# Performance work log

Measured on AMD Instinct MI355X. Metric: run time of the kernel, lower is better.

The kernel has to match this reference:

```python
import jax, jax.numpy as jnp
import numpy as np

# Complete 4-ary tree, leaves at depth 8, heap layout (children of i are 4i+1..4i+4).
B_ARY = 4
DEPTH = 8          # depths 0..8, leaves at depth 8
H = 512            # hidden_channels
IN = 512           # in_channels
OUT = 256          # out_channels
L = 2              # num_layers
LEVEL_STARTS = np.array([(B_ARY ** d - 1) // (B_ARY - 1) for d in range(DEPTH + 2)])
N = int(LEVEL_STARTS[-1])  # 87381


def setup_inputs() -> dict:
    key = jax.random.key(0)
    ks = jax.random.split(key, 12)
    x = jax.random.normal(ks[0], (N, IN), jnp.float32)

    # tree structure (numpy, deterministic)
    n_internal = int(LEVEL_STARTS[DEPTH])
    child_idx = np.zeros((N, B_ARY), np.int32)
    child_mask = np.zeros((N, B_ARY), np.int32)
    internal = np.arange(n_internal)
    child_idx[:n_internal] = (internal[:, None] * B_ARY + 1 + np.arange(B_ARY)[None, :]).astype(np.int32)
    child_mask[:n_internal] = 1
    node_parent = np.full(N, -1, np.int64)
    node_parent[1:] = (np.arange(1, N) - 1) // B_ARY
    node_depth = np.zeros(N, np.int64)
    for d in range(DEPTH + 1):
        node_depth[LEVEL_STARTS[d]:LEVEL_STARTS[d + 1]] = d
    is_leaf = node_depth == DEPTH
    edge_index = np.stack([np.arange(1, N), node_parent[1:]]).astype(np.int64)
    batch = np.zeros(N, np.int64)

    s = 0.02
    params = dict(
        W_in=jax.random.normal(ks[1], (IN, H), jnp.float32) * s,
        b_in=jnp.zeros((H,), jnp.float32),
        W_ioux=jax.random.normal(ks[2], (L, H, 3 * H), jnp.float32) * s,
        b_ioux=jnp.zeros((L, 3 * H), jnp.float32),
        W_iouh=jax.random.normal(ks[3], (L, H, 3 * H), jnp.float32) * s,
        b_iouh=jnp.zeros((L, 3 * H), jnp.float32),
        W_fx=jax.random.normal(ks[4], (L, H, H), jnp.float32) * s,
        b_fx=jnp.zeros((L, H), jnp.float32),
        W_fh=jax.random.normal(ks[5], (L, H, H), jnp.float32) * s,
        b_fh=jnp.zeros((L, H), jnp.float32),
        W_out=jax.random.normal(ks[6], (H, OUT), jnp.float32) * s,
        b_out=jnp.zeros((OUT,), jnp.float32),
    )
    return dict(
        x=x,
        edge_index=jnp.asarray(edge_index),
        batch=jnp.asarray(batch),
        node_depth=jnp.asarray(node_depth),
        node_parent=jnp.asarray(node_parent),
        is_leaf=jnp.asarray(is_leaf),
        child_idx=jnp.asarray(child_idx),
        child_mask=jnp.asarray(child_mask),
        **params,
    )


def reference(x, edge_index, batch, node_depth, node_parent, is_leaf,
              child_idx, child_mask,
              W_in, b_in, W_ioux, b_ioux, W_iouh, b_iouh,
              W_fx, b_fx, W_fh, b_fh, W_out, b_out):
    cm = child_mask.astype(x.dtype)  # [N, B]
    h = jax.nn.relu(x @ W_in + b_in)  # input projection (dropout = eval mode identity)
    for l in range(L):
        hidden = jnp.zeros((N, H), x.dtype)
        cell = jnp.zeros((N, H), x.dtype)
        # bottom-up over tree levels; levels are contiguous static slices
        for d in range(DEPTH, -1, -1):
            s, e = int(LEVEL_STARTS[d]), int(LEVEL_STARTS[d + 1])
            xl = h[s:e]                                   # [n_d, H]
            ci = child_idx[s:e]                           # [n_d, B]
            m = cm[s:e][..., None]                        # [n_d, B, 1]
            ch = hidden[ci] * m                           # masked child hidden
            cc = cell[ci] * m                             # masked child cell
            h_sum = ch.sum(axis=1)                        # child-sum
            iou = xl @ W_ioux[l] + b_ioux[l] + h_sum @ W_iouh[l] + b_iouh[l]
            i, o, u = jnp.split(iou, 3, axis=-1)
            i = jax.nn.sigmoid(i)
            o = jax.nn.sigmoid(o)
            u = jnp.tanh(u)
            f = jax.nn.sigmoid((xl @ W_fx[l] + b_fx[l])[:, None, :] + ch @ W_fh[l] + b_fh[l])
            c = i * u + (f * cc).sum(axis=1)
            hl = o * jnp.tanh(c)
            hidden = hidden.at[s:e].set(hl)
            cell = cell.at[s:e].set(c)
        h = hidden
    node_emb = h @ W_out + b_out                          # [N, OUT]
    tree_emb = jax.ops.segment_sum(node_emb, batch, num_segments=1)  # 'sum' aggregation
    return node_emb, tree_emb
```

## Files before the change

### kernel.cpp

```cpp
#include <hip/hip_runtime.h>

typedef __bf16 bf16;
typedef __bf16 bf16x8 __attribute__((ext_vector_type(8)));
typedef float f32x4 __attribute__((ext_vector_type(4)));

#define NN 87381
#define NINT 21845
#define NLEAF 65536
#define LEAF_START 21845

__device__ __forceinline__ float sigmoidf_(float x) {
    return 1.0f / (1.0f + __expf(-x));
}
__device__ __forceinline__ float tanhf_(float x) {
    return 1.0f - 2.0f / (__expf(2.0f * x) + 1.0f);
}

__device__ __forceinline__ void gload_lds16(const bf16* g, bf16* l) {
    __builtin_amdgcn_global_load_lds(
        (const __attribute__((address_space(1))) unsigned int*)g,
        (__attribute__((address_space(3))) unsigned int*)l, 16, 0, 0);
}

__device__ __forceinline__ int xcd_swz(int bid, int nwg) {
    int q = nwg >> 3, r = nwg & 7;
    int x = bid & 7, i = bid >> 3;
    return (x < r ? x * (q + 1) : r * (q + 1) + (x - r) * q) + i;
}

#define SWZ(r, kc) ((((r) << 3) | ((kc) ^ ((r) & 7))) << 3)

__global__ void tconv_kernel(const float* __restrict__ W, bf16* __restrict__ Wt,
                             int NR, int total) {
    int idx = blockIdx.x * 256 + threadIdx.x;
    if (idx >= total) return;
    int n = idx >> 9;
    int k = idx & 511;
    Wt[idx] = (bf16)W[(size_t)k * NR + n];
}

__global__ void convx_kernel(const float* __restrict__ X, bf16* __restrict__ Y, int total4) {
    int idx = blockIdx.x * 256 + threadIdx.x;
    if (idx >= total4) return;
    const float4 f = *reinterpret_cast<const float4*>(X + (size_t)idx * 4);
    bf16 o[4] = {(bf16)f.x, (bf16)f.y, (bf16)f.z, (bf16)f.w};
    *reinterpret_cast<ushort2*>(Y + (size_t)idx * 4 + 0) = *reinterpret_cast<ushort2*>(&o[0]);
    *reinterpret_cast<ushort2*>(Y + (size_t)idx * 4 + 2) = *reinterpret_cast<ushort2*>(&o[2]);
}

#define MFMA_COMPUTE_2x4(As, Bs, acc, wm, wn, lm, quad)                          \
    _Pragma("unroll")                                                            \
    for (int kk = 0; kk < 64; kk += 32) {                                        \
        const int kc_ = (kk >> 3) + quad;                                        \
        bf16x8 areg[2], breg[4];                                                 \
        _Pragma("unroll")                                                        \
        for (int mi = 0; mi < 2; ++mi)                                           \
            areg[mi] = *reinterpret_cast<const bf16x8*>(                         \
                &(As)[SWZ(wm + mi * 16 + lm, kc_)]);                             \
        _Pragma("unroll")                                                        \
        for (int ni = 0; ni < 4; ++ni)                                           \
            breg[ni] = *reinterpret_cast<const bf16x8*>(                         \
                &(Bs)[SWZ(wn + ni * 16 + lm, kc_)]);                             \
        _Pragma("unroll")                                                        \
        for (int mi = 0; mi < 2; ++mi)                                           \
            _Pragma("unroll")                                                    \
            for (int ni = 0; ni < 4; ++ni)                                       \
                acc[mi][ni] = __builtin_amdgcn_mfma_f32_16x16x32_bf16(           \
                    areg[mi], breg[ni], acc[mi][ni], 0, 0, 0);                   \
    }

__global__ __launch_bounds__(512)
void gemm_kernel(const bf16* __restrict__ A, const bf16* __restrict__ Bt,
                 int bstride, int K, int ntiles,
                 float* __restrict__ Cf, bf16* __restrict__ Cb,
                 const float* __restrict__ bias1, const float* __restrict__ bias2,
                 int M, int N, int relu, int swz)
{
    __shared__ __align__(16) bf16 As[2][128 * 64];
    __shared__ __align__(16) bf16 Bs[2][128 * 64];
    const int tid  = threadIdx.x;
    const int wave = tid >> 6;
    const int lane = tid & 63;
    int bid = blockIdx.x;
    if (swz) bid = xcd_swz(bid, (int)gridDim.x);
    const int bm = (bid / ntiles) * 128;
    const int bn = (bid % ntiles) * 128;
    const int wm = (wave & 3) * 32;
    const int wn = (wave >> 2) * 64;
    const int lm   = lane & 15;
    const int quad = lane >> 4;

    f32x4 acc[2][4];
#pragma unroll
    for (int i = 0; i < 2; ++i)
#pragma unroll
        for (int j = 0; j < 4; ++j) acc[i][j] = (f32x4){0.f, 0.f, 0.f, 0.f};

    const bf16* aptr[2];
    const bf16* bptr[2];
    int loff[2];
#pragma unroll
    for (int i = 0; i < 2; ++i) {
        int c   = i * 512 + tid;
        int r   = c >> 3;
        int kc8 = ((c & 7) ^ (r & 7)) << 3;
        int gr  = bm + r; gr = (gr < M) ? gr : (M - 1);
        aptr[i] = A + (size_t)gr * K + kc8;
        bptr[i] = Bt + (size_t)(bn + r) * bstride + kc8;
        loff[i] = c << 3;
    }

    auto stage = [&](int buf, int t) {
        const int kofs = t << 6;
#pragma unroll
        for (int i = 0; i < 2; ++i)
            gload_lds16(aptr[i] + kofs, &As[0][0] + buf * (128 * 64) + loff[i]);
#pragma unroll
        for (int i = 0; i < 2; ++i)
            gload_lds16(bptr[i] + kofs, &Bs[0][0] + buf * (128 * 64) + loff[i]);
    };

    const int nk = K >> 6;
    stage(0, 0);
    __syncthreads();
    int cur = 0;
    for (int t = 0; t < nk; ++t) {
        if (t + 1 < nk) stage(cur ^ 1, t + 1);
        MFMA_COMPUTE_2x4(As[cur], Bs[cur], acc, wm, wn, lm, quad);
        __syncthreads();
        cur ^= 1;
    }

#pragma unroll
    for (int ni = 0; ni < 4; ++ni) {
        int col = bn + wn + ni * 16 + lm;
        float bsum = (bias1 ? bias1[col] : 0.f) + (bias2 ? bias2[col] : 0.f);
#pragma unroll
        for (int mi = 0; mi < 2; ++mi) {
#pragma unroll
            for (int r = 0; r < 4; ++r) {
                int row = bm + wm + mi * 16 + quad * 4 + r;
                if (row < M) {
                    float v = acc[mi][ni][r] + bsum;
                    if (relu) v = (v > 0.f) ? v : 0.f;
                    if (Cf) Cf[(size_t)row * N + col] = v;
                    else    Cb[(size_t)row * N + col] = (bf16)v;
                }
            }
        }
    }
}

__global__ __launch_bounds__(512)
void leaf_kernel(const bf16* __restrict__ A, const bf16* __restrict__ wiou,
                 const float* __restrict__ bx1, const float* __restrict__ bx2,
                 bf16* __restrict__ hout, bf16* __restrict__ cellout,
                 bf16* __restrict__ hsout, int M, int swz)
{
    __shared__ __align__(16) bf16 As[2][128 * 64];
    __shared__ __align__(16) bf16 Bs[2][3 * 64 * 64];
    const int tid  = threadIdx.x;
    const int wave = tid >> 6;
    const int lane = tid & 63;
    int bid = blockIdx.x;
    if (swz) bid = xcd_swz(bid, (int)gridDim.x);
    const int bm = (bid >> 3) * 128;
    const int bn = (bid & 7) * 64;
    if (bm >= M) return;
    const int wm   = (wave & 3) * 32;
    const int wn   = (wave >> 2) * 32;
    const int lm   = lane & 15;
    const int quad = lane >> 4;

    f32x4 acc[3][2][2];
#pragma unroll
    for (int g = 0; g < 3; ++g)
#pragma unroll
        for (int i = 0; i < 2; ++i)
#pragma unroll
            for (int j = 0; j < 2; ++j) acc[g][i][j] = (f32x4){0.f, 0.f, 0.f, 0.f};

    const bf16* aptr[2];
    int aoff[2];
#pragma unroll
    for (int i = 0; i < 2; ++i) {
        int c   = i * 512 + tid;
        int r   = c >> 3;
        int kc8 = ((c & 7) ^ (r & 7)) << 3;
        int gr  = bm + r; gr = (gr < M) ? gr : (M - 1);
        aptr[i] = A + ((size_t)gr << 9) + kc8;
        aoff[i] = c << 3;
    }
    const bf16* bptr[3];
    int boff[3];
#pragma unroll
    for (int i = 0; i < 3; ++i) {
        int c   = i * 512 + tid;
        int g   = c >> 9;
        int cg  = c & 511;
        int r   = cg >> 3;
        int kc8 = ((cg & 7) ^ (r & 7)) << 3;
        bptr[i] = wiou + (size_t)(g * 512 + bn + r) * 512 + kc8;
        boff[i] = c << 3;
    }

    auto stage = [&](int buf, int t) {
        const int kofs = t << 6;
#pragma unroll
        for (int i = 0; i < 2; ++i)
            gload_lds16(aptr[i] + kofs, &As[0][0] + buf * (128 * 64) + aoff[i]);
#pragma unroll
        for (int i = 0; i < 3; ++i)
            gload_lds16(bptr[i] + kofs, &Bs[0][0] + buf * (3 * 64 * 64) + boff[i]);
    };

    stage(0, 0);
    __syncthreads();
    int cur = 0;
    for (int t = 0; t < 8; ++t) {
        if (t + 1 < 8) stage(cur ^ 1, t + 1);
#pragma unroll
        for (int kk = 0; kk < 64; kk += 32) {
            const int kc_ = (kk >> 3) + quad;
            bf16x8 areg[2];
#pragma unroll
            for (int mi = 0; mi < 2; ++mi)
                areg[mi] = *reinterpret_cast<const bf16x8*>(
                    &As[cur][SWZ(wm + mi * 16 + lm, kc_)]);
            bf16x8 breg[3][2];
#pragma unroll
            for (int g = 0; g < 3; ++g)
#pragma unroll
                for (int ni = 0; ni < 2; ++ni)
                    breg[g][ni] = *reinterpret_cast<const bf16x8*>(
                        &Bs[cur][g * 4096 + SWZ(wn + ni * 16 + lm, kc_)]);
#pragma unroll
            for (int g = 0; g < 3; ++g)
#pragma unroll
                for (int mi = 0; mi < 2; ++mi)
#pragma unroll
                    for (int ni = 0; ni < 2; ++ni)
                        acc[g][mi][ni] = __builtin_amdgcn_mfma_f32_16x16x32_bf16(
                            areg[mi], breg[g][ni], acc[g][mi][ni], 0, 0, 0);
        }
        __syncthreads();
        cur ^= 1;
    }

#pragma unroll
    for (int ni = 0; ni < 2; ++ni) {
        int col = bn + wn + ni * 16 + lm;
        float bi = bx1[col]        + bx2[col];
        float bo = bx1[col + 512]  + bx2[col + 512];
        float bu = bx1[col + 1024] + bx2[col + 1024];
#pragma unroll
        for (int mi = 0; mi < 2; ++mi) {
            int rbase = bm + wm + mi * 16 + quad * 4;
            float hsum = 0.f;
#pragma unroll
            for (int r = 0; r < 4; ++r) {
                int row = rbase + r;
                if (row < M) {
                    float i_ = sigmoidf_(acc[0][mi][ni][r] + bi);
                    float o_ = sigmoidf_(acc[1][mi][ni][r] + bo);
                    float u_ = tanhf_(acc[2][mi][ni][r] + bu);
                    float c  = i_ * u_;
                    bf16 hb  = (bf16)(o_ * tanhf_(c));
                    cellout[(size_t)row * 512 + col] = (bf16)c;
                    hout[(size_t)row * 512 + col] = hb;
                    hsum += (float)hb;
                }
            }
            if (hsout && rbase < M)
                hsout[(size_t)(rbase >> 2) * 512 + col] = (bf16)hsum;
        }
    }
}

__global__ __launch_bounds__(512)
void iou_fused_kernel(const bf16* __restrict__ A, const bf16* __restrict__ wiou,
                      const float* __restrict__ bx1, const float* __restrict__ bx2,
                      const float* __restrict__ fcs, const bf16* __restrict__ xout,
                      bf16* __restrict__ hout, bf16* __restrict__ cellout,
                      bf16* __restrict__ hsout,
                      int M, int swz)
{
    __shared__ __align__(16) bf16 As[2][128 * 64];
    __shared__ __align__(16) bf16 Bs[2][3 * 64 * 64];
    const int tid  = threadIdx.x;
    const int wave = tid >> 6;
    const int lane = tid & 63;
    int bid = blockIdx.x;
    if (swz) bid = xcd_swz(bid, (int)gridDim.x);
    const int bm = (bid >> 3) * 128;
    const int bn = (bid & 7) * 64;
    if (bm >= M) return;
    const int wm   = (wave & 3) * 32;
    const int wn   = (wave >> 2) * 32;
    const int lm   = lane & 15;
    const int quad = lane >> 4;

    f32x4 acc[3][2][2];
#pragma unroll
    for (int g = 0; g < 3; ++g)
#pragma unroll
        for (int i = 0; i < 2; ++i)
#pragma unroll
            for (int j = 0; j < 2; ++j) acc[g][i][j] = (f32x4){0.f, 0.f, 0.f, 0.f};

    const bf16* aptr[2];
    int aoff[2];
#pragma unroll
    for (int i = 0; i < 2; ++i) {
        int c   = i * 512 + tid;
        int r   = c >> 3;
        int kc8 = ((c & 7) ^ (r & 7)) << 3;
        int gr  = bm + r; gr = (gr < M) ? gr : (M - 1);
        aptr[i] = A + ((size_t)gr << 9) + kc8;
        aoff[i] = c << 3;
    }
    const bf16* bptr[3];
    int boff[3];
#pragma unroll
    for (int i = 0; i < 3; ++i) {
        int c   = i * 512 + tid;
        int g   = c >> 9;
        int cg  = c & 511;
        int r   = cg >> 3;
        int kc8 = ((cg & 7) ^ (r & 7)) << 3;
        bptr[i] = wiou + (size_t)(g * 512 + bn + r) * 512 + kc8;
        boff[i] = c << 3;
    }

    auto stage = [&](int buf, int t) {
        const int kofs = t << 6;
#pragma unroll
        for (int i = 0; i < 2; ++i)
            gload_lds16(aptr[i] + kofs, &As[0][0] + buf * (128 * 64) + aoff[i]);
#pragma unroll
        for (int i = 0; i < 3; ++i)
            gload_lds16(bptr[i] + kofs, &Bs[0][0] + buf * (3 * 64 * 64) + boff[i]);
    };

    stage(0, 0);
    __syncthreads();
    int cur = 0;
    for (int t = 0; t < 8; ++t) {
        if (t + 1 < 8) stage(cur ^ 1, t + 1);
#pragma unroll
        for (int kk = 0; kk < 64; kk += 32) {
            const int kc_ = (kk >> 3) + quad;
            bf16x8 areg[2];
#pragma unroll
            for (int mi = 0; mi < 2; ++mi)
                areg[mi] = *reinterpret_cast<const bf16x8*>(
                    &As[cur][SWZ(wm + mi * 16 + lm, kc_)]);
            bf16x8 breg[3][2];
#pragma unroll
            for (int g = 0; g < 3; ++g)
#pragma unroll
                for (int ni = 0; ni < 2; ++ni)
                    breg[g][ni] = *reinterpret_cast<const bf16x8*>(
                        &Bs[cur][g * 4096 + SWZ(wn + ni * 16 + lm, kc_)]);
#pragma unroll
            for (int g = 0; g < 3; ++g)
#pragma unroll
                for (int mi = 0; mi < 2; ++mi)
#pragma unroll
                    for (int ni = 0; ni < 2; ++ni)
                        acc[g][mi][ni] = __builtin_amdgcn_mfma_f32_16x16x32_bf16(
                            areg[mi], breg[g][ni], acc[g][mi][ni], 0, 0, 0);
        }
        __syncthreads();
        cur ^= 1;
    }

#pragma unroll
    for (int ni = 0; ni < 2; ++ni) {
        int col = bn + wn + ni * 16 + lm;
        float bi = bx1[col]        + bx2[col];
        float bo = bx1[col + 512]  + bx2[col + 512];
        float bu = bx1[col + 1024] + bx2[col + 1024];
#pragma unroll
        for (int mi = 0; mi < 2; ++mi) {
            int rbase = bm + wm + mi * 16 + quad * 4;
            float hsum = 0.f;
#pragma unroll
            for (int r = 0; r < 4; ++r) {
                int row = rbase + r;
                if (row < M) {
                    float ax  = (float)xout[(size_t)row * 2048 + col];
                    float aox = (float)xout[(size_t)row * 2048 + 512 + col];
                    float aux = (float)xout[(size_t)row * 2048 + 1024 + col];
                    float i_ = sigmoidf_(acc[0][mi][ni][r] + ax + bi);
                    float o_ = sigmoidf_(acc[1][mi][ni][r] + aox + bo);
                    float u_ = tanhf_(acc[2][mi][ni][r] + aux + bu);
                    float c  = i_ * u_ + fcs[(size_t)row * 512 + col];
                    bf16 hb  = (bf16)(o_ * tanhf_(c));
                    cellout[(size_t)row * 512 + col] = (bf16)c;
                    hout[(size_t)row * 512 + col] = hb;
                    hsum += (float)hb;
                }
            }
            if (hsout && rbase < M)
                hsout[(size_t)(rbase >> 2) * 512 + col] = (bf16)hsum;
        }
    }
}

__global__ __launch_bounds__(512)
void cf_kernel(const bf16* __restrict__ hc, const bf16* __restrict__ cellc,
               const bf16* __restrict__ wfh, const bf16* __restrict__ xout,
               const float* __restrict__ bf1, const float* __restrict__ bf2,
               float* __restrict__ fcs, int E, int swz)
{
    const int M = 4 * E;
    __shared__ __align__(16) bf16 As[2][128 * 64];
    __shared__ __align__(16) bf16 Bs[2][128 * 64];
    const int tid  = threadIdx.x;
    const int wave = tid >> 6;
    const int lane = tid & 63;
    int bid = blockIdx.x;
    if (swz) bid = xcd_swz(bid, (int)gridDim.x);
    const int bm = (bid >> 2) * 128;
    const int bn = (bid & 3) * 128;
    if (bm >= M) return;
    const int wm   = (wave & 3) * 32;
    const int wn   = (wave >> 2) * 64;
    const int lm   = lane & 15;
    const int quad = lane >> 4;

    f32x4 acc[2][4];
#pragma unroll
    for (int i = 0; i < 2; ++i)
#pragma unroll
        for (int j = 0; j < 4; ++j) acc[i][j] = (f32x4){0.f, 0.f, 0.f, 0.f};

    const bf16* aptr[2];
    const bf16* bptr[2];
    int loff[2];
#pragma unroll
    for (int i = 0; i < 2; ++i) {
        int c   = i * 512 + tid;
        int r   = c >> 3;
        int kc8 = ((c & 7) ^ (r & 7)) << 3;
        int gr  = bm + r; gr = (gr < M) ? gr : (M - 1);
        aptr[i] = hc + ((size_t)gr << 9) + kc8;
        bptr[i] = wfh + (size_t)(bn + r) * 512 + kc8;
        loff[i] = c << 3;
    }

    auto stage = [&](int buf, int t) {
        const int kofs = t << 6;
#pragma unroll
        for (int i = 0; i < 2; ++i)
            gload_lds16(aptr[i] + kofs, &As[0][0] + buf * (128 * 64) + loff[i]);
#pragma unroll
        for (int i = 0; i < 2; ++i)
            gload_lds16(bptr[i] + kofs, &Bs[0][0] + buf * (128 * 64) + loff[i]);
    };

    stage(0, 0);
    __syncthreads();
    int cur = 0;
    for (int t = 0; t < 8; ++t) {
        if (t + 1 < 8) stage(cur ^ 1, t + 1);
        MFMA_COMPUTE_2x4(As[cur], Bs[cur], acc, wm, wn, lm, quad);
        __syncthreads();
        cur ^= 1;
    }

#pragma unroll
    for (int ni = 0; ni < 4; ++ni) {
        int col = bn + wn + ni * 16 + lm;
        float bsum = bf1[col] + bf2[col];
#pragma unroll
        for (int mi = 0; mi < 2; ++mi) {
            int R0 = bm + wm + mi * 16;
            if (R0 + quad * 4 < M) {
                int p = (R0 >> 2) + quad;
                float pf = (float)xout[(size_t)p * 2048 + 1536 + col] + bsum;
                float fc = 0.f;
#pragma unroll
                for (int r = 0; r < 4; ++r) {
                    int row = R0 + quad * 4 + r;
                    fc += sigmoidf_(acc[mi][ni][r] + pf) *
                          (float)cellc[(size_t)row * 512 + col];
                }
                fcs[(size_t)p * 512 + col] = fc;
            }
        }
    }
}

#define R1_BLOCKS 2048
#define R1_ROWS 43
__global__ void reduce1_kernel(const float* __restrict__ ne, float* __restrict__ partial)
{
    int t = threadIdx.x;
    int b = blockIdx.x;
    int r0 = b * R1_ROWS;
    int r1 = r0 + R1_ROWS; r1 = (r1 < NN) ? r1 : NN;
    float acc = 0.f;
    for (int r = r0; r < r1; ++r) acc += ne[(size_t)r * 256 + t];
    partial[(size_t)b * 256 + t] = acc;
}
__global__ void reduce2_kernel(const float* __restrict__ partial, float* __restrict__ partial2)
{
    int t = threadIdx.x;
    int b = blockIdx.x;
    float acc = 0.f;
    for (int i = 0; i < 32; ++i) acc += partial[(size_t)(b * 32 + i) * 256 + t];
    partial2[(size_t)b * 256 + t] = acc;
}
__global__ void reduce3_kernel(const float* __restrict__ partial2, float* __restrict__ tree)
{
    int t = threadIdx.x;
    float acc = 0.f;
    for (int i = 0; i < 64; ++i) acc += partial2[(size_t)i * 256 + t];
    tree[t] = acc;
}

extern "C" void kernel_launch(void* const* d_in, const int* in_sizes, int n_in,
                              void* d_out, int out_size, void* d_ws, size_t ws_size,
                              hipStream_t stream)
{
    const float* x      = (const float*)d_in[0];
    const float* W_in   = (const float*)d_in[8];
    const float* b_in   = (const float*)d_in[9];
    const float* W_ioux = (const float*)d_in[10];
    const float* b_ioux = (const float*)d_in[11];
    const float* W_iouh = (const float*)d_in[12];
    const float* b_iouh = (const float*)d_in[13];
    const float* W_fx   = (const float*)d_in[14];
    const float* b_fx   = (const float*)d_in[15];
    const float* W_fh   = (const float*)d_in[16];
    const float* b_fh   = (const float*)d_in[17];
    const float* W_out  = (const float*)d_in[18];
    const float* b_out  = (const float*)d_in[19];

    static const int LS[10] = {0, 1, 5, 21, 85, 341, 1365, 5461, 21845, 87381};

    char* ws = (char*)d_ws;
    size_t off = 0;
    auto take = [&](size_t bytes) -> void* {
        void* p = ws + off;
        off += (bytes + 255) & ~(size_t)255;
        return p;
    };
    bf16*  wt_in      = (bf16*) take((size_t)512 * 512 * 2);
    bf16*  wt_out     = (bf16*) take((size_t)256 * 512 * 2);
    bf16*  wt_xcat    = (bf16*) take((size_t)2 * 2048 * 512 * 2);
    bf16*  wt_iouh    = (bf16*) take((size_t)2 * 1536 * 512 * 2);
    bf16*  wt_fh      = (bf16*) take((size_t)2 * 512 * 512 * 2);
    bf16*  h          = (bf16*) take((size_t)NN * 512 * 2);
    bf16*  hint1      = (bf16*) take((size_t)NINT * 512 * 2);
    bf16*  hB         = (bf16*) take((size_t)NLEAF * 512 * 2);
    bf16*  cell_int   = (bf16*) take((size_t)NINT * 512 * 2);
    bf16*  cell_leaf  = (bf16*) take((size_t)NLEAF * 512 * 2);
    float* fcsum      = (float*)take((size_t)16384 * 512 * 4);
    bf16*  hsA        = (bf16*) take((size_t)16384 * 512 * 2);
    bf16*  hsB        = (bf16*) take((size_t)4096 * 512 * 2);
    bf16*  XOUT       = (bf16*) take((size_t)NINT * 2048 * 2);
    float* partial    = (float*)take((size_t)R1_BLOCKS * 256 * 4);
    float* partial2   = (float*)take((size_t)64 * 256 * 4);
    bf16*  xbf        = cell_int;

    dim3 blk(256), blk512(512);
    auto tgrid = [](int total) { return dim3((unsigned)((total + 255) / 256)); };

    tconv_kernel<<<tgrid(512 * 512), blk, 0, stream>>>(W_in, wt_in, 512, 512 * 512);
    tconv_kernel<<<tgrid(256 * 512), blk, 0, stream>>>(W_out, wt_out, 256, 256 * 512);
    for (int l = 0; l < 2; ++l) {
        bf16* xc = wt_xcat + (size_t)l * 2048 * 512;
        tconv_kernel<<<tgrid(1536 * 512), blk, 0, stream>>>(
            W_ioux + (size_t)l * 512 * 1536, xc, 1536, 1536 * 512);
        tconv_kernel<<<tgrid(512 * 512), blk, 0, stream>>>(
            W_fx + (size_t)l * 512 * 512, xc + (size_t)1536 * 512, 512, 512 * 512);
        tconv_kernel<<<tgrid(1536 * 512), blk, 0, stream>>>(
            W_iouh + (size_t)l * 512 * 1536, wt_iouh + (size_t)l * 1536 * 512,
            1536, 1536 * 512);
        tconv_kernel<<<tgrid(512 * 512), blk, 0, stream>>>(
            W_fh + (size_t)l * 512 * 512, wt_fh + (size_t)l * 512 * 512,
            512, 512 * 512);
    }

    auto gemm = [&](const bf16* A, const bf16* Bt, int bstride, int K,
                    float* Cf, bf16* Cb, const float* b1, const float* b2,
                    int M, int N, int relu, int swz) {
        int mt = (M + 127) / 128, nt = N / 128;
        gemm_kernel<<<dim3((unsigned)(mt * nt)), blk512, 0, stream>>>(
            A, Bt, bstride, K, nt, Cf, Cb, b1, b2, M, N, relu, swz);
    };

    convx_kernel<<<tgrid(NN * 128), blk, 0, stream>>>(x, xbf, NN * 128);
    gemm(xbf, wt_in, 512, 512, nullptr, h, b_in, nullptr, NN, 512, 1, 1);

    for (int l = 0; l < 2; ++l) {
        const bf16* wxc  = wt_xcat + (size_t)l * 2048 * 512;
        const bf16* wih  = wt_iouh + (size_t)l * 1536 * 512;
        const bf16* wfh  = wt_fh + (size_t)l * 512 * 512;
        const float* bx1 = b_ioux + (size_t)l * 1536;
        const float* bx2 = b_iouh + (size_t)l * 1536;
        const float* bf1 = b_fx + (size_t)l * 512;
        const float* bf2 = b_fh + (size_t)l * 512;

        const bf16* lin   = (l == 0) ? (h + (size_t)LEAF_START * 512) : hB;
        bf16*       lout  = (l == 0) ? hB : (h + (size_t)LEAF_START * 512);
        const bf16* hprev = (l == 0) ? h : hint1;
        bf16*       hcur  = (l == 0) ? hint1 : h;

        gemm(hprev, wxc, 512, 512, nullptr, XOUT, nullptr, nullptr,
             NINT, 2048, 0, 1);

        {
            int mt = NLEAF / 128;
            leaf_kernel<<<dim3((unsigned)(mt * 8)), blk512, 0, stream>>>(
                lin, wxc , bx1, bx2,
                lout, cell_leaf, hsA, NLEAF, 1);
        }

        for (int d = 7; d >= 0; --d) {
            int s  = LS[d];
            int E  = LS[d + 1] - LS[d];
            int cs = LS[d + 1];
            const bf16* hc = (d == 7) ? lout : (hcur + (size_t)cs * 512);
            const bf16* cc = (d == 7) ? cell_leaf : (cell_int + (size_t)cs * 512);
            bf16* hs_read  = (d & 1) ? hsA : hsB;
            bf16* hs_write = (d == 0) ? nullptr : ((d & 1) ? hsB : hsA);
            const bf16* xo = XOUT + (size_t)s * 2048;

            int mt_cf = (4 * E + 127) / 128;
            cf_kernel<<<dim3((unsigned)(mt_cf * 4)), blk512, 0, stream>>>(
                hc, cc, wfh, xo, bf1, bf2, fcsum, E, 1);

            int mt_iou = (E + 127) / 128;
            iou_fused_kernel<<<dim3((unsigned)(mt_iou * 8)), blk512, 0, stream>>>(
                hs_read, wih, bx1, bx2, fcsum, xo,
                hcur + (size_t)s * 512, cell_int + (size_t)s * 512, hs_write, E, 1);
        }
    }

    float* node_emb = (float*)d_out;
    gemm(h, wt_out, 512, 512, node_emb, nullptr, b_out, nullptr, NN, 256, 0, 1);
    reduce1_kernel<<<dim3(R1_BLOCKS), blk, 0, stream>>>(node_emb, partial);
    reduce2_kernel<<<dim3(64), blk, 0, stream>>>(partial, partial2);
    reduce3_kernel<<<dim3(1), blk, 0, stream>>>(partial2, node_emb + (size_t)NN * 256);
}
```

Measured before the change: 1.673 ms.

## Merge weight prep, fuse small tree levels, fold tree-sum reduction into output GEMM

Ten weight transpose/convert launches become one table-driven kernel. For tree depths 0–3, the separate forget-gate and iou kernels are replaced by one small kernel that computes both in sequence within each block. The output GEMM now accumulates per-tile column sums through an LDS atomic buffer, so a single final kernel produces the tree embedding instead of three reduction passes that re-read the whole node embedding. The aim is to cut launch overhead and extra memory traffic, at the cost of very low parallelism (8 blocks) on the small levels and an extra epilogue sync in the GEMM.

```diff
diff --git a/kernel.cpp b/kernel.cpp
--- a/kernel.cpp
+++ b/kernel.cpp
@@ -8,6 +8,7 @@
 #define NINT 21845
 #define NLEAF 65536
 #define LEAF_START 21845
+#define MT_OUT 683
 
 __device__ __forceinline__ float sigmoidf_(float x) {
     return 1.0f / (1.0f + __expf(-x));
@@ -30,13 +31,26 @@
 
 #define SWZ(r, kc) ((((r) << 3) | ((kc) ^ ((r) & 7))) << 3)
 
-__global__ void tconv_kernel(const float* __restrict__ W, bf16* __restrict__ Wt,
-                             int NR, int total) {
+struct PrepJobs {
+    const float* src[10];
+    bf16*        dst[10];
+    int          nr[10];
+    int          off[11];
+};
+
+__global__ void tconv_all_kernel(PrepJobs P) {
     int idx = blockIdx.x * 256 + threadIdx.x;
-    if (idx >= total) return;
-    int n = idx >> 9;
-    int k = idx & 511;
-    Wt[idx] = (bf16)W[(size_t)k * NR + n];
+    if (idx >= P.off[10]) return;
+#pragma unroll
+    for (int j = 0; j < 10; ++j) {
+        if (idx < P.off[j + 1]) {
+            int lo = idx - P.off[j];
+            int n  = lo >> 9;
+            int k  = lo & 511;
+            P.dst[j][lo] = (bf16)P.src[j][(size_t)k * P.nr[j] + n];
+            return;
+        }
+    }
 }
 
 __global__ void convx_kernel(const float* __restrict__ X, bf16* __restrict__ Y, int total4) {
@@ -74,6 +88,7 @@
                  int bstride, int K, int ntiles,
                  float* __restrict__ Cf, bf16* __restrict__ Cb,
                  const float* __restrict__ bias1, const float* __restrict__ bias2,
+                 float* __restrict__ colsum,
                  int M, int N, int relu, int swz)
 {
     __shared__ __align__(16) bf16 As[2][128 * 64];
@@ -131,6 +146,7 @@
         cur ^= 1;
     }
 
+    float csum[4] = {0.f, 0.f, 0.f, 0.f};
 #pragma unroll
     for (int ni = 0; ni < 4; ++ni) {
         int col = bn + wn + ni * 16 + lm;
@@ -145,10 +161,32 @@
                     if (relu) v = (v > 0.f) ? v : 0.f;
                     if (Cf) Cf[(size_t)row * N + col] = v;
                     else    Cb[(size_t)row * N + col] = (bf16)v;
+                    csum[ni] += v;
                 }
             }
         }
     }
+
+    if (colsum) {
+        float* cbuf = reinterpret_cast<float*>(&As[0][0]);
+        if (tid < 128) cbuf[tid] = 0.f;
+        __syncthreads();
+#pragma unroll
+        for (int ni = 0; ni < 4; ++ni)
+            atomicAdd(&cbuf[wn + ni * 16 + lm], csum[ni]);
+        __syncthreads();
+        if (tid < 128)
+            colsum[(size_t)(bm >> 7) * N + bn + tid] = cbuf[tid];
+    }
+}
+
+__global__ void reduce_final_kernel(const float* __restrict__ partial,
+                                    float* __restrict__ tree, int mt)
+{
+    int t = threadIdx.x;
+    float a = 0.f;
+    for (int i = 0; i < mt; ++i) a += partial[(size_t)i * 256 + t];
+    tree[t] = a;
 }
 
 __global__ __launch_bounds__(512)
@@ -493,32 +531,225 @@
     }
 }
 
-#define R1_BLOCKS 2048
-#define R1_ROWS 43
-__global__ void reduce1_kernel(const float* __restrict__ ne, float* __restrict__ partial)
+__global__ __launch_bounds__(512)
+void level_small_kernel(const bf16* __restrict__ hs, const bf16* __restrict__ hc,
+                        const bf16* __restrict__ cellc,
+                        const bf16* __restrict__ wih, const bf16* __restrict__ wfh,
+                        const bf16* __restrict__ xout,
+                        const float* __restrict__ bx1, const float* __restrict__ bx2,
+                        const float* __restrict__ bf1, const float* __restrict__ bf2,
+                        float* __restrict__ fcsum,
+                        bf16* __restrict__ hout, bf16* __restrict__ cellout,
+                        bf16* __restrict__ hsout, int E)
 {
-    int t = threadIdx.x;
-    int b = blockIdx.x;
-    int r0 = b * R1_ROWS;
-    int r1 = r0 + R1_ROWS; r1 = (r1 < NN) ? r1 : NN;
-    float acc = 0.f;
-    for (int r = r0; r < r1; ++r) acc += ne[(size_t)r * 256 + t];
-    partial[(size_t)b * 256 + t] = acc;
-}
-__global__ void reduce2_kernel(const float* __restrict__ partial, float* __restrict__ partial2)
-{
-    int t = threadIdx.x;
-    int b = blockIdx.x;
-    float acc = 0.f;
-    for (int i = 0; i < 32; ++i) acc += partial[(size_t)(b * 32 + i) * 256 + t];
-    partial2[(size_t)b * 256 + t] = acc;
-}
-__global__ void reduce3_kernel(const float* __restrict__ partial2, float* __restrict__ tree)
-{
-    int t = threadIdx.x;
-    float acc = 0.f;
-    for (int i = 0; i < 64; ++i) acc += partial2[(size_t)i * 256 + t];
-    tree[t] = acc;
+    __shared__ __align__(16) bf16 As[2][128 * 64];
+    __shared__ __align__(16) bf16 Bs[2][3 * 64 * 64];
+    const int tid  = threadIdx.x;
+    const int wave = tid >> 6;
+    const int lane = tid & 63;
+    const int bm = ((int)blockIdx.x >> 3) * 128;
+    const int bn = (int)blockIdx.x & 7;
+    if (bm >= E) return;
+    const int lm   = lane & 15;
+    const int quad = lane >> 4;
+    const int M4   = 4 * E;
+    const int ns   = (M4 - 4 * bm + 127) >> 7;
+    const int nsc  = (ns < 4) ? ns : 4;
+
+    {
+        const int wmA = (wave & 3) * 32;
+        const int wnA = (wave >> 2) * 32;
+        const int rb  = tid >> 3;
+        const int kcb = ((tid & 7) ^ (rb & 7)) << 3;
+        const bf16* bfp = wfh + (size_t)(bn * 64 + rb) * 512 + kcb;
+        const int  bofs = tid << 3;
+
+        for (int s = 0; s < nsc; ++s) {
+            const bf16* aptrA[2]; int aoffA[2];
+#pragma unroll
+            for (int i = 0; i < 2; ++i) {
+                int c   = i * 512 + tid;
+                int r   = c >> 3;
+                int kc8 = ((c & 7) ^ (r & 7)) << 3;
+                int gr  = 4 * bm + 128 * s + r; gr = (gr < M4) ? gr : (M4 - 1);
+                aptrA[i] = hc + ((size_t)gr << 9) + kc8;
+                aoffA[i] = c << 3;
+            }
+            f32x4 accA[2][2];
+#pragma unroll
+            for (int i = 0; i < 2; ++i)
+#pragma unroll
+                for (int j = 0; j < 2; ++j) accA[i][j] = (f32x4){0.f, 0.f, 0.f, 0.f};
+
+            auto stageA = [&](int buf, int t) {
+                const int kofs = t << 6;
+#pragma unroll
+                for (int i = 0; i < 2; ++i)
+                    gload_lds16(aptrA[i] + kofs, &As[0][0] + buf * (128 * 64) + aoffA[i]);
+                gload_lds16(bfp + kofs, &Bs[0][0] + buf * (3 * 64 * 64) + bofs);
+            };
+
+            stageA(0, 0);
+            __syncthreads();
+            int cur = 0;
+            for (int t = 0; t < 8; ++t) {
+                if (t + 1 < 8) stageA(cur ^ 1, t + 1);
+#pragma unroll
+                for (int kk = 0; kk < 64; kk += 32) {
+                    const int kc_ = (kk >> 3) + quad;
+                    bf16x8 ar[2], br[2];
+#pragma unroll
+                    for (int mi = 0; mi < 2; ++mi)
+                        ar[mi] = *reinterpret_cast<const bf16x8*>(
+                            &As[cur][SWZ(wmA + mi * 16 + lm, kc_)]);
+#pragma unroll
+                    for (int ni = 0; ni < 2; ++ni)
+                        br[ni] = *reinterpret_cast<const bf16x8*>(
+                            &Bs[cur][SWZ(wnA + ni * 16 + lm, kc_)]);
+#pragma unroll
+                    for (int mi = 0; mi < 2; ++mi)
+#pragma unroll
+                        for (int ni = 0; ni < 2; ++ni)
+                            accA[mi][ni] = __builtin_amdgcn_mfma_f32_16x16x32_bf16(
+                                ar[mi], br[ni], accA[mi][ni], 0, 0, 0);
+                }
+                __syncthreads();
+                cur ^= 1;
+            }
+#pragma unroll
+            for (int ni = 0; ni < 2; ++ni) {
+                int col = bn * 64 + wnA + ni * 16 + lm;
+                float bsum = bf1[col] + bf2[col];
+#pragma unroll
+                for (int mi = 0; mi < 2; ++mi) {
+                    int lr = 128 * s + wmA + mi * 16 + quad * 4;
+                    int p  = bm + (lr >> 2);
+                    if (p < E) {
+                        float pf = (float)xout[(size_t)p * 2048 + 1536 + col] + bsum;
+                        float fc = 0.f;
+#pragma unroll
+                        for (int r = 0; r < 4; ++r) {
+                            int cr = 4 * bm + lr + r;
+                            fc += sigmoidf_(accA[mi][ni][r] + pf) *
+                                  (float)cellc[(size_t)cr * 512 + col];
+                        }
+                        fcsum[(size_t)p * 512 + col] = fc;
+                    }
+                }
+            }
+        }
+    }
+
+    const int wm = (wave & 3) * 32;
+    const int wn = (wave >> 2) * 32;
+    const int bncol = bn * 64;
+
+    f32x4 acc[3][2][2];
+#pragma unroll
+    for (int g = 0; g < 3; ++g)
+#pragma unroll
+        for (int i = 0; i < 2; ++i)
+#pragma unroll
+            for (int j = 0; j < 2; ++j) acc[g][i][j] = (f32x4){0.f, 0.f, 0.f, 0.f};
+
+    const bf16* aptr[2];
+    int aoff[2];
+#pragma unroll
+    for (int i = 0; i < 2; ++i) {
+        int c   = i * 512 + tid;
+        int r   = c >> 3;
+        int kc8 = ((c & 7) ^ (r & 7)) << 3;
+        int gr  = bm + r; gr = (gr < E) ? gr : (E - 1);
+        aptr[i] = hs + ((size_t)gr << 9) + kc8;
+        aoff[i] = c << 3;
+    }
+    const bf16* bptr[3];
+    int boff[3];
+#pragma unroll
+    for (int i = 0; i < 3; ++i) {
+        int c   = i * 512 + tid;
+        int g   = c >> 9;
+        int cg  = c & 511;
+        int r   = cg >> 3;
+        int kc8 = ((cg & 7) ^ (r & 7)) << 3;
+        bptr[i] = wih + (size_t)(g * 512 + bncol + r) * 512 + kc8;
+        boff[i] = c << 3;
+    }
+
+    auto stage = [&](int buf, int t) {
+        const int kofs = t << 6;
+#pragma unroll
+        for (int i = 0; i < 2; ++i)
+            gload_lds16(aptr[i] + kofs, &As[0][0] + buf * (128 * 64) + aoff[i]);
+#pragma unroll
+        for (int i = 0; i < 3; ++i)
+            gload_lds16(bptr[i] + kofs, &Bs[0][0] + buf * (3 * 64 * 64) + boff[i]);
+    };
+
+    stage(0, 0);
+    __syncthreads();
+    int cur = 0;
+    for (int t = 0; t < 8; ++t) {
+        if (t + 1 < 8) stage(cur ^ 1, t + 1);
+#pragma unroll
+        for (int kk = 0; kk < 64; kk += 32) {
+            const int kc_ = (kk >> 3) + quad;
+            bf16x8 areg[2];
+#pragma unroll
+            for (int mi = 0; mi < 2; ++mi)
+                areg[mi] = *reinterpret_cast<const bf16x8*>(
+                    &As[cur][SWZ(wm + mi * 16 + lm, kc_)]);
+            bf16x8 breg[3][2];
+#pragma unroll
+            for (int g = 0; g < 3; ++g)
+#pragma unroll
+                for (int ni = 0; ni < 2; ++ni)
+                    breg[g][ni] = *reinterpret_cast<const bf16x8*>(
+                        &Bs[cur][g * 4096 + SWZ(wn + ni * 16 + lm, kc_)]);
+#pragma unroll
+            for (int g = 0; g < 3; ++g)
+#pragma unroll
+                for (int mi = 0; mi < 2; ++mi)
+#pragma unroll
+                    for (int ni = 0; ni < 2; ++ni)
+                        acc[g][mi][ni] = __builtin_amdgcn_mfma_f32_16x16x32_bf16(
+                            areg[mi], breg[g][ni], acc[g][mi][ni], 0, 0, 0);
+        }
+        __syncthreads();
+        cur ^= 1;
+    }
+
+#pragma unroll
+    for (int ni = 0; ni < 2; ++ni) {
+        int col = bncol + wn + ni * 16 + lm;
+        float bi = bx1[col]        + bx2[col];
+        float bo = bx1[col + 512]  + bx2[col + 512];
+        float bu = bx1[col + 1024] + bx2[col + 1024];
+#pragma unroll
+        for (int mi = 0; mi < 2; ++mi) {
+            int rbase = bm + wm + mi * 16 + quad * 4;
+            float hsum = 0.f;
+#pragma unroll
+            for (int r = 0; r < 4; ++r) {
+                int row = rbase + r;
+                if (row < E) {
+                    float ax  = (float)xout[(size_t)row * 2048 + col];
+                    float aox = (float)xout[(size_t)row * 2048 + 512 + col];
+                    float aux = (float)xout[(size_t)row * 2048 + 1024 + col];
+                    float i_ = sigmoidf_(acc[0][mi][ni][r] + ax + bi);
+                    float o_ = sigmoidf_(acc[1][mi][ni][r] + aox + bo);
+                    float u_ = tanhf_(acc[2][mi][ni][r] + aux + bu);
+                    float c  = i_ * u_ + fcsum[(size_t)row * 512 + col];
+                    bf16 hb  = (bf16)(o_ * tanhf_(c));
+                    cellout[(size_t)row * 512 + col] = (bf16)c;
+                    hout[(size_t)row * 512 + col] = hb;
+                    hsum += (float)hb;
+                }
+            }
+            if (hsout && rbase < E)
+                hsout[(size_t)(rbase >> 2) * 512 + col] = (bf16)hsum;
+        }
+    }
 }
 
 extern "C" void kernel_launch(void* const* d_in, const int* in_sizes, int n_in,
@@ -562,39 +793,41 @@
     bf16*  hsA        = (bf16*) take((size_t)16384 * 512 * 2);
     bf16*  hsB        = (bf16*) take((size_t)4096 * 512 * 2);
     bf16*  XOUT       = (bf16*) take((size_t)NINT * 2048 * 2);
-    float* partial    = (float*)take((size_t)R1_BLOCKS * 256 * 4);
-    float* partial2   = (float*)take((size_t)64 * 256 * 4);
+    float* partial    = (float*)take((size_t)MT_OUT * 256 * 4);
     bf16*  xbf        = cell_int;
 
     dim3 blk(256), blk512(512);
     auto tgrid = [](int total) { return dim3((unsigned)((total + 255) / 256)); };
 
-    tconv_kernel<<<tgrid(512 * 512), blk, 0, stream>>>(W_in, wt_in, 512, 512 * 512);
-    tconv_kernel<<<tgrid(256 * 512), blk, 0, stream>>>(W_out, wt_out, 256, 256 * 512);
-    for (int l = 0; l < 2; ++l) {
-        bf16* xc = wt_xcat + (size_t)l * 2048 * 512;
-        tconv_kernel<<<tgrid(1536 * 512), blk, 0, stream>>>(
-            W_ioux + (size_t)l * 512 * 1536, xc, 1536, 1536 * 512);
-        tconv_kernel<<<tgrid(512 * 512), blk, 0, stream>>>(
-            W_fx + (size_t)l * 512 * 512, xc + (size_t)1536 * 512, 512, 512 * 512);
-        tconv_kernel<<<tgrid(1536 * 512), blk, 0, stream>>>(
-            W_iouh + (size_t)l * 512 * 1536, wt_iouh + (size_t)l * 1536 * 512,
-            1536, 1536 * 512);
-        tconv_kernel<<<tgrid(512 * 512), blk, 0, stream>>>(
-            W_fh + (size_t)l * 512 * 512, wt_fh + (size_t)l * 512 * 512,
-            512, 512 * 512);
+    {
+        PrepJobs P;
+        int o = 0, j = 0;
+        auto add = [&](const float* s, bf16* d, int nr, int tot) {
+            P.src[j] = s; P.dst[j] = d; P.nr[j] = nr; P.off[j] = o; o += tot; ++j;
+        };
+        add(W_in,  wt_in,  512, 512 * 512);
+        add(W_out, wt_out, 256, 256 * 512);
+        for (int l = 0; l < 2; ++l) {
+            bf16* xc = wt_xcat + (size_t)l * 2048 * 512;
+            add(W_ioux + (size_t)l * 512 * 1536, xc,                       1536, 1536 * 512);
+            add(W_fx   + (size_t)l * 512 * 512,  xc + (size_t)1536 * 512,  512,  512 * 512);
+            add(W_iouh + (size_t)l * 512 * 1536, wt_iouh + (size_t)l * 1536 * 512, 1536, 1536 * 512);
+            add(W_fh   + (size_t)l * 512 * 512,  wt_fh + (size_t)l * 512 * 512,    512,  512 * 512);
+        }
+        P.off[10] = o;
+        tconv_all_kernel<<<tgrid(o), blk, 0, stream>>>(P);
     }
 
     auto gemm = [&](const bf16* A, const bf16* Bt, int bstride, int K,
                     float* Cf, bf16* Cb, const float* b1, const float* b2,
-                    int M, int N, int relu, int swz) {
+                    float* colsum, int M, int N, int relu, int swz) {
         int mt = (M + 127) / 128, nt = N / 128;
         gemm_kernel<<<dim3((unsigned)(mt * nt)), blk512, 0, stream>>>(
-            A, Bt, bstride, K, nt, Cf, Cb, b1, b2, M, N, relu, swz);
+            A, Bt, bstride, K, nt, Cf, Cb, b1, b2, colsum, M, N, relu, swz);
     };
 
     convx_kernel<<<tgrid(NN * 128), blk, 0, stream>>>(x, xbf, NN * 128);
-    gemm(xbf, wt_in, 512, 512, nullptr, h, b_in, nullptr, NN, 512, 1, 1);
+    gemm(xbf, wt_in, 512, 512, nullptr, h, b_in, nullptr, nullptr, NN, 512, 1, 1);
 
     for (int l = 0; l < 2; ++l) {
         const bf16* wxc  = wt_xcat + (size_t)l * 2048 * 512;
@@ -610,14 +843,13 @@
         const bf16* hprev = (l == 0) ? h : hint1;
         bf16*       hcur  = (l == 0) ? hint1 : h;
 
-        gemm(hprev, wxc, 512, 512, nullptr, XOUT, nullptr, nullptr,
+        gemm(hprev, wxc, 512, 512, nullptr, XOUT, nullptr, nullptr, nullptr,
              NINT, 2048, 0, 1);
 
         {
             int mt = NLEAF / 128;
             leaf_kernel<<<dim3((unsigned)(mt * 8)), blk512, 0, stream>>>(
-                lin, wxc , bx1, bx2,
-                lout, cell_leaf, hsA, NLEAF, 1);
+                lin, wxc, bx1, bx2, lout, cell_leaf, hsA, NLEAF, 1);
         }
 
         for (int d = 7; d >= 0; --d) {
@@ -630,20 +862,26 @@
             bf16* hs_write = (d == 0) ? nullptr : ((d & 1) ? hsB : hsA);
             const bf16* xo = XOUT + (size_t)s * 2048;
 
-            int mt_cf = (4 * E + 127) / 128;
-            cf_kernel<<<dim3((unsigned)(mt_cf * 4)), blk512, 0, stream>>>(
-                hc, cc, wfh, xo, bf1, bf2, fcsum, E, 1);
-
-            int mt_iou = (E + 127) / 128;
-            iou_fused_kernel<<<dim3((unsigned)(mt_iou * 8)), blk512, 0, stream>>>(
-                hs_read, wih, bx1, bx2, fcsum, xo,
-                hcur + (size_t)s * 512, cell_int + (size_t)s * 512, hs_write, E, 1);
+            if (d >= 4) {
+                int mt_cf = (4 * E + 127) / 128;
+                cf_kernel<<<dim3((unsigned)(mt_cf * 4)), blk512, 0, stream>>>(
+                    hc, cc, wfh, xo, bf1, bf2, fcsum, E, 1);
+
+                int mt_iou = (E + 127) / 128;
+                iou_fused_kernel<<<dim3((unsigned)(mt_iou * 8)), blk512, 0, stream>>>(
+                    hs_read, wih, bx1, bx2, fcsum, xo,
+                    hcur + (size_t)s * 512, cell_int + (size_t)s * 512, hs_write, E, 1);
+            } else {
+                level_small_kernel<<<dim3(8u), blk512, 0, stream>>>(
+                    hs_read, hc, cc, wih, wfh, xo, bx1, bx2, bf1, bf2, fcsum,
+                    hcur + (size_t)s * 512, cell_int + (size_t)s * 512, hs_write, E);
+            }
         }
     }
 
     float* node_emb = (float*)d_out;
-    gemm(h, wt_out, 512, 512, node_emb, nullptr, b_out, nullptr, NN, 256, 0, 1);
-    reduce1_kernel<<<dim3(R1_BLOCKS), blk, 0, stream>>>(node_emb, partial);
-    reduce2_kernel<<<dim3(64), blk, 0, stream>>>(partial, partial2);
-    reduce3_kernel<<<dim3(1), blk, 0, stream>>>(partial2, node_emb + (size_t)NN * 256);
-}
+    gemm(h, wt_out, 512, 512, node_emb, nullptr, b_out, nullptr, partial,
+         NN, 256, 0, 1);
+    reduce_final_kernel<<<dim3(1), blk, 0, stream>>>(
+        partial, node_emb + (size_t)NN * 256, MT_OUT);
+}
```

New measurement: 1.771 ms. +5.9%, slower.
